# Kernel tuning notes

Hardware: AMD Instinct MI355X
Metric: run time of the kernel (lower is better)

## Reference

```python
import jax, jax.numpy as jnp
import numpy as np

K = 5      # kernel_size
STRIDE = 1
EPS = 1e-7


def _extract_patches(x, k, s):
    # x: [B,H,W,C] -> [B,Ho,Wo,k,k,C], same (kh,kw,c) layout as tf.extract_image_patches VALID
    B, H, W, C = x.shape
    Ho = (H - k) // s + 1
    Wo = (W - k) // s + 1
    r = (jnp.arange(Ho) * s)[:, None] + jnp.arange(k)   # [Ho,k]
    c = (jnp.arange(Wo) * s)[:, None] + jnp.arange(k)   # [Wo,k]
    return x[:, r[:, None, :, None], c[None, :, None, :], :]


def _rotate(pflat, angle, k):
    # Replicates tf.contrib.image.transform with angles_to_projective_transforms,
    # including the (1+1e-7) normalization of the 3x3 matrix in the original code.
    # pflat: [N, k*k, C], angle: [N]; bilinear sampling, fill value 0 outside.
    N = pflat.shape[0]
    f32 = pflat.dtype
    co, si = jnp.cos(angle), jnp.sin(angle)
    km1 = jnp.asarray(k - 1, f32)
    xoff = (km1 - (co * km1 - si * km1)) * 0.5
    yoff = (km1 - (si * km1 + co * km1)) * 0.5
    scale = 1.0 / (1.0 + EPS)  # transforms /= transforms[:, 8:9] + 1e-7
    gy, gx = jnp.meshgrid(jnp.arange(k, dtype=f32), jnp.arange(k, dtype=f32), indexing='ij')
    sx = (co[:, None, None] * gx - si[:, None, None] * gy + xoff[:, None, None]) * scale
    sy = (si[:, None, None] * gx + co[:, None, None] * gy + yoff[:, None, None]) * scale
    sx = sx.reshape(N, k * k)
    sy = sy.reshape(N, k * k)
    x0 = jnp.floor(sx)
    y0 = jnp.floor(sy)
    wx = (sx - x0)[..., None]
    wy = (sy - y0)[..., None]
    x0i = x0.astype(jnp.int32)
    y0i = y0.astype(jnp.int32)

    def samp(yi, xi):
        valid = (xi >= 0) & (xi < k) & (yi >= 0) & (yi < k)
        idx = jnp.clip(yi, 0, k - 1) * k + jnp.clip(xi, 0, k - 1)   # [N,k*k]
        v = jnp.take_along_axis(pflat, idx[..., None], axis=1)      # [N,k*k,C]
        return jnp.where(valid[..., None], v, jnp.zeros((), f32))

    v00 = samp(y0i, x0i)
    v01 = samp(y0i, x0i + 1)
    v10 = samp(y0i + 1, x0i)
    v11 = samp(y0i + 1, x0i + 1)
    top = v00 * (1 - wx) + v01 * wx
    bot = v10 * (1 - wx) + v11 * wx
    return top * (1 - wy) + bot * wy   # [N,k*k,C]


def _forward(input_tensor, W, b):
    k, s = K, STRIDE
    B, H, Wd, C = input_tensor.shape
    patches = _extract_patches(input_tensor, k, s)      # [B,Ho,Wo,k,k,C]
    Ho, Wo = patches.shape[1], patches.shape[2]
    inten = patches.sum(-1)                             # [B,Ho,Wo,k,k] channel-sum intensity
    ridx = jnp.arange(k, dtype=patches.dtype)
    tot = inten.sum((-2, -1)) + EPS
    cr = (inten * ridx[:, None]).sum((-2, -1)) / tot    # centroid row
    cc = (inten * ridx[None, :]).sum((-2, -1)) / tot    # centroid col
    m = (k - 1) / 2.0                                   # meanCenter (same for row/col)
    angle = jnp.arctan2(cr - m, cc - m + EPS)           # [B,Ho,Wo]
    pflat = patches.reshape(B * Ho * Wo, k * k, C)
    rot = _rotate(pflat, angle.reshape(-1), k)          # [N,k*k,C]
    rot = rot.reshape(B, Ho * Wo, k * k * C)
    wflat = W.reshape(W.shape[0], -1)                   # [F, k*k*C]
    out = jnp.einsum('bpd,fd->bpf', rot, wflat)         # elementwise-mult-sum 'conv'
    return out.reshape(B, Ho, Wo, -1) + b


def setup_inputs():
    key = jax.random.key(0)
    k1, k2 = jax.random.split(key, 2)
    B, H, Wd, C, F = 4, 128, 128, 16, 32
    input_tensor = jax.random.uniform(k1, (B, H, Wd, C), dtype=jnp.float32)
    lim = float(np.sqrt(6.0 / (K * K * C + F)))  # glorot_uniform
    W = jax.random.uniform(k2, (F, K, K, C), minval=-lim, maxval=lim, dtype=jnp.float32)
    b = jnp.zeros((F,), jnp.float32)
    return {"input_tensor": input_tensor, "W": W, "b": b}


def reference(input_tensor, W, b):
    return _forward(input_tensor, W, b)
```

## Files before the change

### kernel.cpp

```cpp
#include <hip/hip_runtime.h>


#define KS     5
#define TILE   8
#define TW     (TILE + KS - 1)
#define CPAD   20
#define SINH   24
#define C_IN   16
#define F_OUT  32
#define H_IN   128
#define W_IN   128
#define HO     124
#define WO     124
#define NBATCH 4
#define EPSF   1e-7f
#define BLOCK  256
#define KW     400

#define SINT_OFF    11520
#define ANG_OFF     12160
#define SINH_OFF    13184
#define RED_STRIDE  34
#define RED_WAVE    (64 * RED_STRIDE)
#define SMEM_BYTES  34816

typedef _Float16 half8  __attribute__((ext_vector_type(8)));
typedef _Float16 half4v __attribute__((ext_vector_type(4)));
typedef __attribute__((ext_vector_type(4))) float floatx4;

static __device__ __forceinline__ half8 blend8h(
    const _Float16* __restrict__ s_inh, int lxq, int lyq,
    float co, float si, float xo, float yo, int t, int ch0)
{
    const float scl = 1.0f / (1.0f + EPSF);
    int ky = t / KS, kx = t - KS * ky;
    float sx = (co * (float)kx - si * (float)ky + xo) * scl;
    float sy = (si * (float)kx + co * (float)ky + yo) * scl;
    float fx0 = floorf(sx), fy0 = floorf(sy);
    float wx = sx - fx0, wy = sy - fy0;
    int x0 = (int)fx0, y0 = (int)fy0;
    int x1 = x0 + 1, y1 = y0 + 1;
    float vx0 = (x0 >= 0 && x0 < KS) ? 1.f : 0.f;
    float vx1 = (x1 >= 0 && x1 < KS) ? 1.f : 0.f;
    float vy0 = (y0 >= 0 && y0 < KS) ? 1.f : 0.f;
    float vy1 = (y1 >= 0 && y1 < KS) ? 1.f : 0.f;
    float w00 = (1.f - wx) * (1.f - wy) * vx0 * vy0;
    float w01 = wx * (1.f - wy) * vx1 * vy0;
    float w10 = (1.f - wx) * wy * vx0 * vy1;
    float w11 = wx * wy * vx1 * vy1;
    int cx0 = min(max(x0, 0), KS - 1), cx1 = min(max(x1, 0), KS - 1);
    int cy0 = min(max(y0, 0), KS - 1), cy1 = min(max(y1, 0), KS - 1);
    const _Float16* p00 = &s_inh[((lyq + cy0) * TW + (lxq + cx0)) * SINH + ch0];
    const _Float16* p01 = &s_inh[((lyq + cy0) * TW + (lxq + cx1)) * SINH + ch0];
    const _Float16* p10 = &s_inh[((lyq + cy1) * TW + (lxq + cx0)) * SINH + ch0];
    const _Float16* p11 = &s_inh[((lyq + cy1) * TW + (lxq + cx1)) * SINH + ch0];
    half8 a = *(const half8*)p00;
    half8 b = *(const half8*)p01;
    half8 c = *(const half8*)p10;
    half8 d = *(const half8*)p11;
    _Float16 h00 = (_Float16)w00, h01 = (_Float16)w01;
    _Float16 h10 = (_Float16)w10, h11 = (_Float16)w11;
    half8 W00 = {h00,h00,h00,h00,h00,h00,h00,h00};
    half8 W01 = {h01,h01,h01,h01,h01,h01,h01,h01};
    half8 W10 = {h10,h10,h10,h10,h10,h10,h10,h10};
    half8 W11 = {h11,h11,h11,h11,h11,h11,h11,h11};
    return a * W00 + b * W01 + c * W10 + d * W11;
}

__global__ __launch_bounds__(BLOCK, 2) void rotconv_kernel(
    const float* __restrict__ in, const float* __restrict__ Wg,
    const float* __restrict__ bg, float* __restrict__ out)
{
    __shared__ __align__(16) char smem[SMEM_BYTES];
    float*    s_in   = (float*)smem;
    float*    s_int  = (float*)(smem + SINT_OFF);
    float4*   s_ang4 = (float4*)(smem + ANG_OFF);
    _Float16* s_inh  = (_Float16*)(smem + SINH_OFF);
    float*    red    = (float*)smem;

    const int tid  = threadIdx.x;
    const int bx = blockIdx.x, by = blockIdx.y, bimg = blockIdx.z;
    const int ox = bx * TILE, oy = by * TILE;

    const float* inb = in + (size_t)bimg * (H_IN * W_IN * C_IN);
    for (int i = tid; i < TW * TW * (C_IN / 4); i += BLOCK) {
        int cv = i & 3;
        int pp = i >> 2;
        int x = pp % TW, y = pp / TW;
        int gy = oy + y, gx = ox + x;
        float4 v = make_float4(0.f, 0.f, 0.f, 0.f);
        if (gy < H_IN && gx < W_IN)
            v = *(const float4*)(inb + ((size_t)(gy * W_IN + gx) * C_IN) + 4 * cv);
        *(float4*)(&s_in[pp * CPAD + 4 * cv]) = v;
    }
    __syncthreads();

    for (int pp = tid; pp < TW * TW; pp += BLOCK) {
        const float* sp = &s_in[pp * CPAD];
        float s = 0.f;
        #pragma unroll
        for (int c = 0; c < C_IN; ++c) s += sp[c];
        s_int[(pp / TW) * (TW + 1) + (pp % TW)] = s;
    }
    __syncthreads();

    if (tid < 64) {
        const int alx = tid & 7, aly = tid >> 3;
        float tot = EPSF, cr = 0.f, cc = 0.f;
        #pragma unroll
        for (int dy = 0; dy < KS; ++dy)
            #pragma unroll
            for (int dx = 0; dx < KS; ++dx) {
                float v = s_int[(aly + dy) * (TW + 1) + (alx + dx)];
                tot += v; cr += v * (float)dy; cc += v * (float)dx;
            }
        cr /= tot; cc /= tot;
        float ang = atan2f(cr - 2.0f, cc - 2.0f + EPSF);
        float si, co;
        sincosf(ang, &si, &co);
        float xoff = (4.0f - (co * 4.0f - si * 4.0f)) * 0.5f;
        float yoff = (4.0f - (si * 4.0f + co * 4.0f)) * 0.5f;
        s_ang4[tid] = make_float4(co, si, xoff, yoff);
    }
    for (int i = tid; i < TW * TW * (C_IN / 4); i += BLOCK) {
        int cv = i & 3;
        int pp = i >> 2;
        float4 v = *(const float4*)(&s_in[pp * CPAD + 4 * cv]);
        half4v h = {(_Float16)v.x, (_Float16)v.y, (_Float16)v.z, (_Float16)v.w};
        *(half4v*)(&s_inh[pp * SINH + 4 * cv]) = h;
    }
    __syncthreads();

    const int p    = tid & 63;
    const int wv   = tid >> 6;
    const int col  = p & 15;
    const int quad = p >> 4;

    float4 angs[4];
    #pragma unroll
    for (int m = 0; m < 4; ++m) angs[m] = s_ang4[16 * m + col];

    floatx4 acc[4][2];
    #pragma unroll
    for (int m = 0; m < 4; ++m) {
        acc[m][0] = (floatx4){0.f, 0.f, 0.f, 0.f};
        acc[m][1] = acc[m][0];
    }

    const int nstep = (wv == 0) ? 4 : 3;
    const int lxq = col & 7, lyq0 = col >> 3;
    const int ch0 = (quad & 1) * 8;
    const half8 zero8 = {0,0,0,0,0,0,0,0};

    #pragma unroll
    for (int s = 0; s < 4; ++s) {
        if (s < nstep) {
            const int ta = wv + 8 * s;
            const int tb = ta + 4;
            const int tq = (quad < 2) ? ta : tb;

            half8 bf0 = zero8, bf1 = zero8;
            if (tq < KS * KS) {
                const float* wp0 = Wg + (size_t)col * KW + tq * 16 + ch0;
                float4 a = *(const float4*)(wp0);
                float4 b = *(const float4*)(wp0 + 4);
                bf0 = (half8){(_Float16)a.x, (_Float16)a.y, (_Float16)a.z, (_Float16)a.w,
                              (_Float16)b.x, (_Float16)b.y, (_Float16)b.z, (_Float16)b.w};
                const float* wp1 = wp0 + (size_t)16 * KW;
                float4 c = *(const float4*)(wp1);
                float4 d = *(const float4*)(wp1 + 4);
                bf1 = (half8){(_Float16)c.x, (_Float16)c.y, (_Float16)c.z, (_Float16)c.w,
                              (_Float16)d.x, (_Float16)d.y, (_Float16)d.z, (_Float16)d.w};
            }

            #pragma unroll
            for (int m = 0; m < 4; ++m) {
                half8 av = zero8;
                if (tq < KS * KS)
                    av = blend8h(s_inh, lxq, 2 * m + lyq0,
                                 angs[m].x, angs[m].y, angs[m].z, angs[m].w,
                                 tq, ch0);
                acc[m][0] = __builtin_amdgcn_mfma_f32_16x16x32_f16(av, bf0, acc[m][0], 0, 0, 0);
                acc[m][1] = __builtin_amdgcn_mfma_f32_16x16x32_f16(av, bf1, acc[m][1], 0, 0, 0);
            }
        }
    }

    __syncthreads();
    #pragma unroll
    for (int m = 0; m < 4; ++m)
        #pragma unroll
        for (int n = 0; n < 2; ++n)
            #pragma unroll
            for (int r = 0; r < 4; ++r) {
                int px = 16 * m + 4 * quad + r;
                red[wv * RED_WAVE + px * RED_STRIDE + n * 16 + col] = acc[m][n][r];
            }
    __syncthreads();

    const int rpx = tid >> 2;
    const int rf0 = (tid & 3) * 8;
    float sum[8];
    #pragma unroll
    for (int j = 0; j < 8; ++j) sum[j] = bg[rf0 + j];
    #pragma unroll
    for (int w = 0; w < 4; ++w) {
        const float* rp = red + w * RED_WAVE + rpx * RED_STRIDE + rf0;
        #pragma unroll
        for (int j = 0; j < 8; ++j) sum[j] += rp[j];
    }
    const int ho = oy + (rpx >> 3), wo = ox + (rpx & 7);
    if (ho < HO && wo < WO) {
        float* op = out + (((size_t)bimg * HO + ho) * WO + wo) * F_OUT + rf0;
        *(float4*)op       = make_float4(sum[0], sum[1], sum[2], sum[3]);
        *(float4*)(op + 4) = make_float4(sum[4], sum[5], sum[6], sum[7]);
    }
}

extern "C" void kernel_launch(void* const* d_in, const int* in_sizes, int n_in,
                              void* d_out, int out_size, void* d_ws, size_t ws_size,
                              hipStream_t stream) {
    const float* in = (const float*)d_in[0];
    const float* Wg = (const float*)d_in[1];
    const float* bg = (const float*)d_in[2];
    float* out      = (float*)d_out;
    dim3 grid((WO + TILE - 1) / TILE, (HO + TILE - 1) / TILE, NBATCH);
    rotconv_kernel<<<grid, dim3(BLOCK), 0, stream>>>(in, Wg, bg, out);
}
```

Measured before the change: 73.59 us.

## Fuse fp16 staging and channel partial sums into load; replace atan2+sincos

The global load loop now converts each float4 straight to fp16 in shared memory and stores a per-float4 partial channel sum. This removes the fp32 staging buffer, the separate intensity-sum pass and the separate conversion pass, along with one barrier. The angle's cos and sin are now taken as the normalised centroid offset vector instead of calling atan2f and then sincosf. This drops transcendental work, but the result can differ slightly in rounding and needs a special case when the vector is near zero.

Result: faster. 71.43 us, median of 2 (-2.9%).

```diff
diff --git a/kernel.cpp b/kernel.cpp
--- a/kernel.cpp
+++ b/kernel.cpp
@@ -4,7 +4,6 @@
 #define KS     5
 #define TILE   8
 #define TW     (TILE + KS - 1)
-#define CPAD   20
 #define SINH   24
 #define C_IN   16
 #define F_OUT  32
@@ -17,9 +16,8 @@
 #define BLOCK  256
 #define KW     400
 
-#define SINT_OFF    11520
-#define ANG_OFF     12160
-#define SINH_OFF    13184
+#define PART_OFF    6912
+#define ANG_OFF     9216
 #define RED_STRIDE  34
 #define RED_WAVE    (64 * RED_STRIDE)
 #define SMEM_BYTES  34816
@@ -72,10 +70,9 @@
     const float* __restrict__ bg, float* __restrict__ out)
 {
     __shared__ __align__(16) char smem[SMEM_BYTES];
-    float*    s_in   = (float*)smem;
-    float*    s_int  = (float*)(smem + SINT_OFF);
+    _Float16* s_inh  = (_Float16*)smem;
+    float*    s_part = (float*)(smem + PART_OFF);
     float4*   s_ang4 = (float4*)(smem + ANG_OFF);
-    _Float16* s_inh  = (_Float16*)(smem + SINH_OFF);
     float*    red    = (float*)smem;
 
     const int tid  = threadIdx.x;
@@ -91,16 +88,9 @@
         float4 v = make_float4(0.f, 0.f, 0.f, 0.f);
         if (gy < H_IN && gx < W_IN)
             v = *(const float4*)(inb + ((size_t)(gy * W_IN + gx) * C_IN) + 4 * cv);
-        *(float4*)(&s_in[pp * CPAD + 4 * cv]) = v;
-    }
-    __syncthreads();
-
-    for (int pp = tid; pp < TW * TW; pp += BLOCK) {
-        const float* sp = &s_in[pp * CPAD];
-        float s = 0.f;
-        #pragma unroll
-        for (int c = 0; c < C_IN; ++c) s += sp[c];
-        s_int[(pp / TW) * (TW + 1) + (pp % TW)] = s;
+        half4v h = {(_Float16)v.x, (_Float16)v.y, (_Float16)v.z, (_Float16)v.w};
+        *(half4v*)(&s_inh[pp * SINH + 4 * cv]) = h;
+        s_part[pp * 4 + cv] = (v.x + v.y) + (v.z + v.w);
     }
     __syncthreads();
 
@@ -111,23 +101,19 @@
         for (int dy = 0; dy < KS; ++dy)
             #pragma unroll
             for (int dx = 0; dx < KS; ++dx) {
-                float v = s_int[(aly + dy) * (TW + 1) + (alx + dx)];
+                float4 pv = *(const float4*)(&s_part[((aly + dy) * TW + (alx + dx)) * 4]);
+                float v = (pv.x + pv.y) + (pv.z + pv.w);
                 tot += v; cr += v * (float)dy; cc += v * (float)dx;
             }
         cr /= tot; cc /= tot;
-        float ang = atan2f(cr - 2.0f, cc - 2.0f + EPSF);
-        float si, co;
-        sincosf(ang, &si, &co);
+        float dyv = cr - 2.0f, dxv = cc - 2.0f + EPSF;
+        float r = sqrtf(dxv * dxv + dyv * dyv);
+        float co, si;
+        if (r < 1e-20f) { co = 1.f; si = 0.f; }
+        else           { float ri = 1.0f / r; co = dxv * ri; si = dyv * ri; }
         float xoff = (4.0f - (co * 4.0f - si * 4.0f)) * 0.5f;
         float yoff = (4.0f - (si * 4.0f + co * 4.0f)) * 0.5f;
         s_ang4[tid] = make_float4(co, si, xoff, yoff);
-    }
-    for (int i = tid; i < TW * TW * (C_IN / 4); i += BLOCK) {
-        int cv = i & 3;
-        int pp = i >> 2;
-        float4 v = *(const float4*)(&s_in[pp * CPAD + 4 * cv]);
-        half4v h = {(_Float16)v.x, (_Float16)v.y, (_Float16)v.z, (_Float16)v.w};
-        *(half4v*)(&s_inh[pp * SINH + 4 * cv]) = h;
     }
     __syncthreads();
 
```
